# Performance work log

Hardware: AMD Instinct MI355X
Metric: run time of the kernel (lower is better)

## Reference

```python
import jax, jax.numpy as jnp
import numpy as np

OUT, IN = 4096, 4096
PACKED = (OUT * IN + 1) // 2


def setup_inputs() -> dict:
    key = jax.random.key(0)
    k1, k2, k3, k4, k5 = jax.random.split(key, 5)
    x = jax.random.normal(k1, (4, 2048, IN), dtype=jnp.float32)
    weight_packed = jax.random.randint(k2, (PACKED,), 0, 256, dtype=jnp.int32)
    scale = jax.random.uniform(k3, (OUT, 1), dtype=jnp.float32) * 0.01 + 1e-4
    zero_point = jax.random.uniform(k4, (OUT, 1), dtype=jnp.float32) * 8.0
    bias = jax.random.normal(k5, (OUT,), dtype=jnp.float32) * 0.02
    return {"x": x, "weight_packed": weight_packed, "scale": scale,
            "zero_point": zero_point, "bias": bias}


def _dequant_weight(weight_packed, scale, zero_point):
    # Unpack two 4-bit nibbles per byte; low nibble first (matches torch.stack dim=1 + flatten)
    low = (weight_packed & 15).astype(jnp.float32)          # [PACKED]
    high = ((weight_packed >> 4) & 15).astype(jnp.float32)   # [PACKED]
    unpacked = jnp.stack([low, high], axis=1).reshape(-1)     # [2*PACKED]
    w = unpacked[: OUT * IN].reshape(OUT, IN)
    # weight * scale - zero_point * scale == (weight - zero_point) * scale
    return (w - zero_point) * scale                           # [OUT, IN]


def reference(x, weight_packed, scale, zero_point, bias):
    w = _dequant_weight(weight_packed, scale, zero_point)
    # F.linear: x @ w.T + bias
    return jnp.einsum('bsi,oi->bso', x, w) + bias
```

## Files before the change

### kernel.cpp

```cpp
#include <hip/hip_runtime.h>
#include <hip/hip_bf16.h>


typedef __bf16 bf16;
typedef __attribute__((ext_vector_type(8))) __bf16 bf16x8;
typedef __attribute__((ext_vector_type(4))) float f32x4;
typedef __attribute__((ext_vector_type(4))) unsigned int u32x4;

#define OUT_DIM 4096
#define IN_DIM  4096
#define M_DIM   8192

__global__ __launch_bounds__(256) void dequant_w_kernel(
    const int* __restrict__ wp, const float* __restrict__ scale,
    const float* __restrict__ zp, bf16* __restrict__ W)
{
  const int t = blockIdx.x * 256 + threadIdx.x;
  const long j = (long)t * 8;
  const int o = (int)(j >> 12);
  const float s = scale[o];
  const float zs = zp[o] * s;
  const int4 p = *(const int4*)(wp + (long)t * 4);
  const int v[4] = {p.x, p.y, p.z, p.w};
  union { bf16 h[8]; u32x4 u; } r;
#pragma unroll
  for (int q = 0; q < 4; ++q) {
    r.h[2*q]   = (bf16)((float)(v[q] & 15) * s - zs);
    r.h[2*q+1] = (bf16)((float)((v[q] >> 4) & 15) * s - zs);
  }
  *(u32x4*)(W + j) = r.u;
}

__global__ __launch_bounds__(256) void cvt_x_kernel(
    const float* __restrict__ x, bf16* __restrict__ xb)
{
  const long t = (long)blockIdx.x * 256 + threadIdx.x;
  const long i = t * 8;
  const f32x4 a = *(const f32x4*)(x + i);
  const f32x4 b = *(const f32x4*)(x + i + 4);
  union { bf16 h[8]; u32x4 u; } r;
#pragma unroll
  for (int q = 0; q < 4; ++q) { r.h[q] = (bf16)a[q]; r.h[4+q] = (bf16)b[q]; }
  *(u32x4*)(xb + i) = r.u;
}

__global__ __launch_bounds__(512, 2) void gemm_bt_bias_kernel(
    const bf16* __restrict__ A, const bf16* __restrict__ B,
    const float* __restrict__ bias, float* __restrict__ C)
{
  const int N = OUT_DIM, K = IN_DIM;
  const int NT = IN_DIM / 64;

  __shared__ bf16 sm[2][4][256][32];

  const int bid = blockIdx.x;
  const int swz = (bid & 7) * (512 / 8) + (bid >> 3);
  const int bm = swz >> 4;
  const int bn = swz & 15;

  const int tid  = threadIdx.x;
  const int wave = tid >> 6;
  const int lane = tid & 63;
  const int wr = wave >> 2;
  const int wc = wave & 3;

  const long row0 = (long)bm * 256;
  const long col0 = (long)bn * 256;

  const int L0 = tid * 16;
  const int L1 = 8192 + tid * 16;
  const int Lw0 = L0 ^ (((L0 >> 9) & 1) << 5);
  const int Lw1 = L1 ^ (((L1 >> 9) & 1) << 5);
  const int sr0 = Lw0 >> 6, sc0 = (Lw0 & 63) >> 1;
  const int sr1 = Lw1 >> 6, sc1 = (Lw1 & 63) >> 1;
  const bf16* a0 = A + (row0 + sr0) * (long)K + sc0;
  const bf16* a1 = A + (row0 + sr1) * (long)K + sc1;
  const bf16* b0 = B + (col0 + sr0) * (long)K + sc0;
  const bf16* b1 = B + (col0 + sr1) * (long)K + sc1;

#define STAGE(P0, P1, HALF, KOFF) do {                                          \
    __builtin_amdgcn_global_load_lds(                                           \
        (const __attribute__((address_space(1))) void*)((P0) + (KOFF)),         \
        (__attribute__((address_space(3))) void*)((char*)(HALF) + L0), 16, 0, 0);\
    __builtin_amdgcn_global_load_lds(                                           \
        (const __attribute__((address_space(1))) void*)((P1) + (KOFF)),         \
        (__attribute__((address_space(3))) void*)((char*)(HALF) + L1), 16, 0, 0);\
  } while (0)

  const int lane15 = lane & 15;
  const int rb = (lane15 * 64 + ((lane >> 4) << 4)) ^ ((lane & 8) << 2);
  const int wrB = wr * 8192;
  const int wcB = wc * 4096;

  f32x4 acc[8][4] = {};

#define PHASE(BUF, KS, STAGE_STMT, VM_STMT) do {                                \
    VM_STMT;                                                                    \
    __builtin_amdgcn_s_barrier();                                               \
    asm volatile("" ::: "memory");            \
    const char* Ab = (const char*)&sm[BUF][KS][0][0];                           \
    const char* Bb = (const char*)&sm[BUF][2 + (KS)][0][0];                     \
    bf16x8 fb[4], fa[8];                                                        \
    _Pragma("unroll")                                                           \
    for (int f = 0; f < 4; ++f) fb[f] = *(const bf16x8*)(Bb + wcB + f*1024 + rb); \
    _Pragma("unroll")                                                           \
    for (int f = 0; f < 8; ++f) fa[f] = *(const bf16x8*)(Ab + wrB + f*1024 + rb); \
    STAGE_STMT;                                                                 \
    __builtin_amdgcn_s_setprio(1);                                              \
    _Pragma("unroll")                                                           \
    for (int i = 0; i < 8; ++i)                                                 \
      _Pragma("unroll")                                                         \
      for (int j = 0; j < 4; ++j)                                               \
        acc[i][j] = __builtin_amdgcn_mfma_f32_16x16x32_bf16(fa[i], fb[j], acc[i][j], 0, 0, 0); \
    __builtin_amdgcn_s_setprio(0);                                              \
  } while (0)

  STAGE(a0, a1, &sm[0][0][0][0], 0);
  STAGE(b0, b1, &sm[0][2][0][0], 0);
  STAGE(a0, a1, &sm[0][1][0][0], 32);
  STAGE(b0, b1, &sm[0][3][0][0], 32);

  for (int T = 0; T < NT; ++T) {
    const int buf = T & 1;
    const int nbuf = buf ^ 1;
    const int nko = (T + 1) * 64;
    const bool st = (T + 1 < NT);

    PHASE(buf, 0,
          { if (st) { STAGE(a0, a1, &sm[nbuf][0][0][0], nko);
                      STAGE(b0, b1, &sm[nbuf][2][0][0], nko); } },
          { asm volatile("s_waitcnt vmcnt(4)" ::: "memory"); });
    PHASE(buf, 1,
          { if (st) { STAGE(a0, a1, &sm[nbuf][1][0][0], nko + 32);
                      STAGE(b0, b1, &sm[nbuf][3][0][0], nko + 32); } },
          { if (T == NT - 1) asm volatile("s_waitcnt vmcnt(0)" ::: "memory");
            else             asm volatile("s_waitcnt vmcnt(4)" ::: "memory"); });
  }

  const long cr0 = row0 + wr * 128 + ((lane >> 4) << 2);
  const long cc0 = col0 + wc * 64 + lane15;
#pragma unroll
  for (int j = 0; j < 4; ++j) {
    const long gc = cc0 + j * 16;
    const float bv = bias[gc];
#pragma unroll
    for (int mf = 0; mf < 8; ++mf) {
      float* cp = C + (cr0 + mf * 16) * (long)N + gc;
#pragma unroll
      for (int r = 0; r < 4; ++r)
        cp[(long)r * N] = acc[mf][j][r] + bv;
    }
  }
#undef PHASE
#undef STAGE
}

extern "C" void kernel_launch(void* const* d_in, const int* in_sizes, int n_in,
                              void* d_out, int out_size, void* d_ws, size_t ws_size,
                              hipStream_t stream)
{
  const float* x     = (const float*)d_in[0];
  const int*   wp    = (const int*)d_in[1];
  const float* scale = (const float*)d_in[2];
  const float* zp    = (const float*)d_in[3];
  const float* bias  = (const float*)d_in[4];
  float* out = (float*)d_out;

  bf16* Wb = (bf16*)d_ws;
  bf16* Xb = (bf16*)((char*)d_ws + (size_t)OUT_DIM * IN_DIM * 2);

  dequant_w_kernel<<<(OUT_DIM * (long)IN_DIM / 8) / 256, 256, 0, stream>>>(wp, scale, zp, Wb);
  cvt_x_kernel<<<(M_DIM * (long)IN_DIM / 8) / 256, 256, 0, stream>>>(x, Xb);
  gemm_bt_bias_kernel<<<512, 512, 0, stream>>>(Xb, Wb, bias, out);
}
```

Before: 281.9 us.

## Software-pipeline LDS fragment reads with register double-buffering in GEMM loop

The GEMM main loop now reads the next half-tile's A/B fragments from LDS into a second register set while MFMAs run on the current set. Global-to-LDS staging is rescheduled so each half-buffer is refilled as soon as its fragments have been read. The aim is to hide LDS read latency behind the matrix instructions. The extra fragment registers raise register pressure, which could hurt occupancy under the 512x2 launch bounds.

```diff
diff --git a/kernel.cpp b/kernel.cpp
--- a/kernel.cpp
+++ b/kernel.cpp
@@ -93,25 +93,25 @@
   const int wcB = wc * 4096;
 
   f32x4 acc[8][4] = {};
+  bf16x8 pa[8], pb[4];
+  bf16x8 qa[8], qb[4];
 
-#define PHASE(BUF, KS, STAGE_STMT, VM_STMT) do {                                \
-    VM_STMT;                                                                    \
-    __builtin_amdgcn_s_barrier();                                               \
-    asm volatile("" ::: "memory");            \
+#define RD(RA, RB, BUF, KS) do {                                                \
     const char* Ab = (const char*)&sm[BUF][KS][0][0];                           \
     const char* Bb = (const char*)&sm[BUF][2 + (KS)][0][0];                     \
-    bf16x8 fb[4], fa[8];                                                        \
     _Pragma("unroll")                                                           \
-    for (int f = 0; f < 4; ++f) fb[f] = *(const bf16x8*)(Bb + wcB + f*1024 + rb); \
+    for (int f = 0; f < 4; ++f) RB[f] = *(const bf16x8*)(Bb + wcB + f*1024 + rb); \
     _Pragma("unroll")                                                           \
-    for (int f = 0; f < 8; ++f) fa[f] = *(const bf16x8*)(Ab + wrB + f*1024 + rb); \
-    STAGE_STMT;                                                                 \
+    for (int f = 0; f < 8; ++f) RA[f] = *(const bf16x8*)(Ab + wrB + f*1024 + rb); \
+  } while (0)
+
+#define MFMAS(CA, CB) do {                                                      \
     __builtin_amdgcn_s_setprio(1);                                              \
     _Pragma("unroll")                                                           \
     for (int i = 0; i < 8; ++i)                                                 \
       _Pragma("unroll")                                                         \
       for (int j = 0; j < 4; ++j)                                               \
-        acc[i][j] = __builtin_amdgcn_mfma_f32_16x16x32_bf16(fa[i], fb[j], acc[i][j], 0, 0, 0); \
+        acc[i][j] = __builtin_amdgcn_mfma_f32_16x16x32_bf16(CA[i], CB[j], acc[i][j], 0, 0, 0); \
     __builtin_amdgcn_s_setprio(0);                                              \
   } while (0)
 
@@ -119,22 +119,37 @@
   STAGE(b0, b1, &sm[0][2][0][0], 0);
   STAGE(a0, a1, &sm[0][1][0][0], 32);
   STAGE(b0, b1, &sm[0][3][0][0], 32);
+  asm volatile("s_waitcnt vmcnt(4)" ::: "memory");
+  __builtin_amdgcn_s_barrier();
+  STAGE(a0, a1, &sm[1][0][0][0], 64);
+  STAGE(b0, b1, &sm[1][2][0][0], 64);
+  RD(pa, pb, 0, 0);
 
   for (int T = 0; T < NT; ++T) {
     const int buf = T & 1;
     const int nbuf = buf ^ 1;
-    const int nko = (T + 1) * 64;
-    const bool st = (T + 1 < NT);
+    const bool st1 = (T + 1 < NT);
+    const bool st2 = (T + 2 < NT);
 
-    PHASE(buf, 0,
-          { if (st) { STAGE(a0, a1, &sm[nbuf][0][0][0], nko);
-                      STAGE(b0, b1, &sm[nbuf][2][0][0], nko); } },
-          { asm volatile("s_waitcnt vmcnt(4)" ::: "memory"); });
-    PHASE(buf, 1,
-          { if (st) { STAGE(a0, a1, &sm[nbuf][1][0][0], nko + 32);
-                      STAGE(b0, b1, &sm[nbuf][3][0][0], nko + 32); } },
-          { if (T == NT - 1) asm volatile("s_waitcnt vmcnt(0)" ::: "memory");
-            else             asm volatile("s_waitcnt vmcnt(4)" ::: "memory"); });
+    if (st1) asm volatile("s_waitcnt vmcnt(4)" ::: "memory");
+    else     asm volatile("s_waitcnt vmcnt(0)" ::: "memory");
+    __builtin_amdgcn_s_barrier();
+    if (st1) {
+      STAGE(a0, a1, &sm[nbuf][1][0][0], (T + 1) * 64 + 32);
+      STAGE(b0, b1, &sm[nbuf][3][0][0], (T + 1) * 64 + 32);
+    }
+    RD(qa, qb, buf, 1);
+    MFMAS(pa, pb);
+
+    if (st1) asm volatile("s_waitcnt vmcnt(4)" ::: "memory");
+    else     asm volatile("s_waitcnt vmcnt(0)" ::: "memory");
+    __builtin_amdgcn_s_barrier();
+    if (st2) {
+      STAGE(a0, a1, &sm[buf][0][0][0], (T + 2) * 64);
+      STAGE(b0, b1, &sm[buf][2][0][0], (T + 2) * 64);
+    }
+    if (st1) RD(pa, pb, nbuf, 0);
+    MFMAS(qa, qb);
   }
 
   const long cr0 = row0 + wr * 128 + ((lane >> 4) << 2);
@@ -151,7 +166,8 @@
         cp[(long)r * N] = acc[mf][j][r] + bv;
     }
   }
-#undef PHASE
+#undef RD
+#undef MFMAS
 #undef STAGE
 }
 
```

Result: slower. 291.4 us (+3.4%).

## Fuse weight dequantization into GEMM with packed 4-bit LDS staging

Applied to the files above, without the earlier changes.

Removes the standalone bf16 weight dequant kernel. A small repack kernel now compresses the int32-per-byte weights into dense packed bytes. The GEMM loads those 4-bit nibbles into LDS with 4-byte global_load_lds and dequantizes them to bf16 fragments in registers, using per-column scale and zero-point held in registers, just before the MFMAs. This cuts weight write/read traffic and LDS footprint, at the cost of extra VALU work in the MFMA inner loop. That unpack work is also repeated by the waves that share the same columns.

```diff
diff --git a/kernel.cpp b/kernel.cpp
--- a/kernel.cpp
+++ b/kernel.cpp
@@ -10,26 +10,6 @@
 #define OUT_DIM 4096
 #define IN_DIM  4096
 #define M_DIM   8192
-
-__global__ __launch_bounds__(256) void dequant_w_kernel(
-    const int* __restrict__ wp, const float* __restrict__ scale,
-    const float* __restrict__ zp, bf16* __restrict__ W)
-{
-  const int t = blockIdx.x * 256 + threadIdx.x;
-  const long j = (long)t * 8;
-  const int o = (int)(j >> 12);
-  const float s = scale[o];
-  const float zs = zp[o] * s;
-  const int4 p = *(const int4*)(wp + (long)t * 4);
-  const int v[4] = {p.x, p.y, p.z, p.w};
-  union { bf16 h[8]; u32x4 u; } r;
-#pragma unroll
-  for (int q = 0; q < 4; ++q) {
-    r.h[2*q]   = (bf16)((float)(v[q] & 15) * s - zs);
-    r.h[2*q+1] = (bf16)((float)((v[q] >> 4) & 15) * s - zs);
-  }
-  *(u32x4*)(W + j) = r.u;
-}
 
 __global__ __launch_bounds__(256) void cvt_x_kernel(
     const float* __restrict__ x, bf16* __restrict__ xb)
@@ -44,14 +24,31 @@
   *(u32x4*)(xb + i) = r.u;
 }
 
+__global__ __launch_bounds__(256) void repack_w_kernel(
+    const int* __restrict__ wp, unsigned int* __restrict__ wb)
+{
+  const long t = (long)blockIdx.x * 256 + threadIdx.x;
+  const long e = t * 16;
+  u32x4 r;
+#pragma unroll
+  for (int q = 0; q < 4; ++q) {
+    const int4 p = *(const int4*)(wp + e + q * 4);
+    r[q] = (unsigned)(p.x & 255) | ((unsigned)(p.y & 255) << 8) |
+           ((unsigned)(p.z & 255) << 16) | ((unsigned)(p.w & 255) << 24);
+  }
+  *(u32x4*)(wb + t * 4) = r;
+}
+
 __global__ __launch_bounds__(512, 2) void gemm_bt_bias_kernel(
-    const bf16* __restrict__ A, const bf16* __restrict__ B,
+    const bf16* __restrict__ A, const unsigned char* __restrict__ WP,
+    const float* __restrict__ scale, const float* __restrict__ zp,
     const float* __restrict__ bias, float* __restrict__ C)
 {
   const int N = OUT_DIM, K = IN_DIM;
   const int NT = IN_DIM / 64;
 
-  __shared__ bf16 sm[2][4][256][32];
+  __shared__ bf16 smA[2][2][256][32];
+  __shared__ unsigned int smB[2][2][256][4];
 
   const int bid = blockIdx.x;
   const int swz = (bid & 7) * (512 / 8) + (bid >> 3);
@@ -75,37 +72,65 @@
   const int sr1 = Lw1 >> 6, sc1 = (Lw1 & 63) >> 1;
   const bf16* a0 = A + (row0 + sr0) * (long)K + sc0;
   const bf16* a1 = A + (row0 + sr1) * (long)K + sc1;
-  const bf16* b0 = B + (col0 + sr0) * (long)K + sc0;
-  const bf16* b1 = B + (col0 + sr1) * (long)K + sc1;
 
-#define STAGE(P0, P1, HALF, KOFF) do {                                          \
+  const int brow  = tid >> 2;
+  const int bbyte = (tid & 3) * 4;
+  const unsigned char* w0 = WP + (col0 + brow) * 2048L + bbyte;
+  const unsigned char* w1 = WP + (col0 + brow + 128) * 2048L + bbyte;
+
+#define STAGE_G(BUF, KS, KOFF) do {                                             \
+    char* Ah = (char*)&smA[BUF][KS][0][0];                                      \
+    char* Bh = (char*)&smB[BUF][KS][0][0];                                      \
     __builtin_amdgcn_global_load_lds(                                           \
-        (const __attribute__((address_space(1))) void*)((P0) + (KOFF)),         \
-        (__attribute__((address_space(3))) void*)((char*)(HALF) + L0), 16, 0, 0);\
+        (const __attribute__((address_space(1))) void*)(a0 + (KOFF)),           \
+        (__attribute__((address_space(3))) void*)(Ah + L0), 16, 0, 0);          \
     __builtin_amdgcn_global_load_lds(                                           \
-        (const __attribute__((address_space(1))) void*)((P1) + (KOFF)),         \
-        (__attribute__((address_space(3))) void*)((char*)(HALF) + L1), 16, 0, 0);\
+        (const __attribute__((address_space(1))) void*)(a1 + (KOFF)),           \
+        (__attribute__((address_space(3))) void*)(Ah + L1), 16, 0, 0);          \
+    __builtin_amdgcn_global_load_lds(                                           \
+        (const __attribute__((address_space(1))) void*)(w0 + ((KOFF) >> 1)),    \
+        (__attribute__((address_space(3))) void*)(Bh + tid * 4), 4, 0, 0);      \
+    __builtin_amdgcn_global_load_lds(                                           \
+        (const __attribute__((address_space(1))) void*)(w1 + ((KOFF) >> 1)),    \
+        (__attribute__((address_space(3))) void*)(Bh + 2048 + tid * 4), 4, 0, 0);\
   } while (0)
 
   const int lane15 = lane & 15;
-  const int rb = (lane15 * 64 + ((lane >> 4) << 4)) ^ ((lane & 8) << 2);
+  const int rb  = (lane15 * 64 + ((lane >> 4) << 4)) ^ ((lane & 8) << 2);
   const int wrB = wr * 8192;
-  const int wcB = wc * 4096;
+  const int rBb = (wc * 64 + lane15) * 16 + ((lane >> 4) << 2);
+
+  float sv[4], zv[4];
+#pragma unroll
+  for (int f = 0; f < 4; ++f) {
+    const int n = (int)col0 + wc * 64 + f * 16 + lane15;
+    sv[f] = scale[n];
+    zv[f] = zp[n] * sv[f];
+  }
 
   f32x4 acc[8][4] = {};
 
 #define PHASE(BUF, KS, STAGE_STMT, VM_STMT) do {                                \
     VM_STMT;                                                                    \
     __builtin_amdgcn_s_barrier();                                               \
-    asm volatile("" ::: "memory");            \
-    const char* Ab = (const char*)&sm[BUF][KS][0][0];                           \
-    const char* Bb = (const char*)&sm[BUF][2 + (KS)][0][0];                     \
-    bf16x8 fb[4], fa[8];                                                        \
+    asm volatile("" ::: "memory");        \
+    const char* Ab = (const char*)&smA[BUF][KS][0][0];                          \
+    const char* Bp = (const char*)&smB[BUF][KS][0][0];                          \
+    unsigned int pk[4];                                                         \
     _Pragma("unroll")                                                           \
-    for (int f = 0; f < 4; ++f) fb[f] = *(const bf16x8*)(Bb + wcB + f*1024 + rb); \
+    for (int f = 0; f < 4; ++f) pk[f] = *(const unsigned int*)(Bp + rBb + f * 256); \
+    bf16x8 fa[8];                                                               \
     _Pragma("unroll")                                                           \
-    for (int f = 0; f < 8; ++f) fa[f] = *(const bf16x8*)(Ab + wrB + f*1024 + rb); \
+    for (int f = 0; f < 8; ++f) fa[f] = *(const bf16x8*)(Ab + wrB + f * 1024 + rb); \
     STAGE_STMT;                                                                 \
+    bf16x8 fb[4];                                                               \
+    _Pragma("unroll")                                                           \
+    for (int f = 0; f < 4; ++f) {                                               \
+      const float fs = sv[f], fz = zv[f];                                       \
+      _Pragma("unroll")                                                         \
+      for (int e = 0; e < 8; ++e)                                               \
+        fb[f][e] = (bf16)((float)((pk[f] >> (4 * e)) & 15u) * fs - fz);         \
+    }                                                                           \
     __builtin_amdgcn_s_setprio(1);                                              \
     _Pragma("unroll")                                                           \
     for (int i = 0; i < 8; ++i)                                                 \
@@ -115,10 +140,8 @@
     __builtin_amdgcn_s_setprio(0);                                              \
   } while (0)
 
-  STAGE(a0, a1, &sm[0][0][0][0], 0);
-  STAGE(b0, b1, &sm[0][2][0][0], 0);
-  STAGE(a0, a1, &sm[0][1][0][0], 32);
-  STAGE(b0, b1, &sm[0][3][0][0], 32);
+  STAGE_G(0, 0, 0);
+  STAGE_G(0, 1, 32);
 
   for (int T = 0; T < NT; ++T) {
     const int buf = T & 1;
@@ -127,12 +150,10 @@
     const bool st = (T + 1 < NT);
 
     PHASE(buf, 0,
-          { if (st) { STAGE(a0, a1, &sm[nbuf][0][0][0], nko);
-                      STAGE(b0, b1, &sm[nbuf][2][0][0], nko); } },
+          { if (st) STAGE_G(nbuf, 0, nko); },
           { asm volatile("s_waitcnt vmcnt(4)" ::: "memory"); });
     PHASE(buf, 1,
-          { if (st) { STAGE(a0, a1, &sm[nbuf][1][0][0], nko + 32);
-                      STAGE(b0, b1, &sm[nbuf][3][0][0], nko + 32); } },
+          { if (st) STAGE_G(nbuf, 1, nko + 32); },
           { if (T == NT - 1) asm volatile("s_waitcnt vmcnt(0)" ::: "memory");
             else             asm volatile("s_waitcnt vmcnt(4)" ::: "memory"); });
   }
@@ -152,7 +173,7 @@
     }
   }
 #undef PHASE
-#undef STAGE
+#undef STAGE_G
 }
 
 extern "C" void kernel_launch(void* const* d_in, const int* in_sizes, int n_in,
@@ -166,10 +187,11 @@
   const float* bias  = (const float*)d_in[4];
   float* out = (float*)d_out;
 
-  bf16* Wb = (bf16*)d_ws;
-  bf16* Xb = (bf16*)((char*)d_ws + (size_t)OUT_DIM * IN_DIM * 2);
+  bf16* Xb = (bf16*)d_ws;
+  unsigned int* Wb = (unsigned int*)((char*)d_ws + 67108864);
 
-  dequant_w_kernel<<<(OUT_DIM * (long)IN_DIM / 8) / 256, 256, 0, stream>>>(wp, scale, zp, Wb);
   cvt_x_kernel<<<(M_DIM * (long)IN_DIM / 8) / 256, 256, 0, stream>>>(x, Xb);
-  gemm_bt_bias_kernel<<<512, 512, 0, stream>>>(Xb, Wb, bias, out);
+  repack_w_kernel<<<(OUT_DIM * (long)IN_DIM / 2 / 16) / 256, 256, 0, stream>>>(wp, Wb);
+  gemm_bt_bias_kernel<<<512, 512, 0, stream>>>(
+      Xb, (const unsigned char*)Wb, scale, zp, bias, out);
 }
```

Result: slower. 335.1 us (+18.9%).

## Switch GEMM to 32x32x16 bf16 MFMA with matching LDS tile layout

Applied to the files above, without the earlier changes.

Replaces the 16x16x32 MFMA tiling with 32x32x16 bf16 MFMA instructions, so each wave holds a 4x2 grid of 32x32 accumulators instead of 8x4 16x16 tiles. The global-to-LDS staging layout and fragment addressing are rewritten so lanes read the operand layout the larger MFMA expects, and the epilogue store mapping is adjusted to match. The larger MFMA issues fewer instructions and reads fewer LDS fragments per FLOP. The new LDS layout drops the previous XOR swizzle, which risks LDS bank conflicts on the fragment reads.

```diff
diff --git a/kernel.cpp b/kernel.cpp
--- a/kernel.cpp
+++ b/kernel.cpp
@@ -5,6 +5,7 @@
 typedef __bf16 bf16;
 typedef __attribute__((ext_vector_type(8))) __bf16 bf16x8;
 typedef __attribute__((ext_vector_type(4))) float f32x4;
+typedef __attribute__((ext_vector_type(16))) float f32x16;
 typedef __attribute__((ext_vector_type(4))) unsigned int u32x4;
 
 #define OUT_DIM 4096
@@ -51,7 +52,8 @@
   const int N = OUT_DIM, K = IN_DIM;
   const int NT = IN_DIM / 64;
 
-  __shared__ bf16 sm[2][4][256][32];
+  __shared__ char smA[2][2][16384];
+  __shared__ char smB[2][2][16384];
 
   const int bid = blockIdx.x;
   const int swz = (bid & 7) * (512 / 8) + (bid >> 3);
@@ -59,66 +61,73 @@
   const int bn = swz & 15;
 
   const int tid  = threadIdx.x;
+  const int lane = tid & 63;
   const int wave = tid >> 6;
-  const int lane = tid & 63;
   const int wr = wave >> 2;
   const int wc = wave & 3;
 
   const long row0 = (long)bm * 256;
   const long col0 = (long)bn * 256;
 
-  const int L0 = tid * 16;
-  const int L1 = 8192 + tid * 16;
-  const int Lw0 = L0 ^ (((L0 >> 9) & 1) << 5);
-  const int Lw1 = L1 ^ (((L1 >> 9) & 1) << 5);
-  const int sr0 = Lw0 >> 6, sc0 = (Lw0 & 63) >> 1;
-  const int sr1 = Lw1 >> 6, sc1 = (Lw1 & 63) >> 1;
-  const bf16* a0 = A + (row0 + sr0) * (long)K + sc0;
-  const bf16* a1 = A + (row0 + sr1) * (long)K + sc1;
-  const bf16* b0 = B + (col0 + sr0) * (long)K + sc0;
-  const bf16* b1 = B + (col0 + sr1) * (long)K + sc1;
+  const int arow = (tid >> 7) * 32 + (tid & 31);
+  const int kadj = ((tid >> 6) & 1) * 16 + ((tid >> 5) & 1) * 8;
+  const bf16* aP0 = A + (row0 + arow) * (long)K + kadj;
+  const bf16* aP1 = aP0 + 128 * (long)K;
+  const bf16* bP0 = B + (col0 + arow) * (long)K + kadj;
+  const bf16* bP1 = bP0 + 128 * (long)K;
+  const int LA = tid * 16;
 
-#define STAGE(P0, P1, HALF, KOFF) do {                                          \
-    __builtin_amdgcn_global_load_lds(                                           \
-        (const __attribute__((address_space(1))) void*)((P0) + (KOFF)),         \
-        (__attribute__((address_space(3))) void*)((char*)(HALF) + L0), 16, 0, 0);\
-    __builtin_amdgcn_global_load_lds(                                           \
-        (const __attribute__((address_space(1))) void*)((P1) + (KOFF)),         \
-        (__attribute__((address_space(3))) void*)((char*)(HALF) + L1), 16, 0, 0);\
+#define GL(P, D) __builtin_amdgcn_global_load_lds(                              \
+      (const __attribute__((address_space(1))) void*)(P),                       \
+      (__attribute__((address_space(3))) void*)(D), 16, 0, 0)
+
+#define STAGE_G(BUF, KS, KOFF) do {                                             \
+    char* Ah = &smA[BUF][KS][0];                                                \
+    char* Bh = &smB[BUF][KS][0];                                                \
+    GL(aP0 + (KOFF), Ah + LA);                                                  \
+    GL(aP1 + (KOFF), Ah + 8192 + LA);                                           \
+    GL(bP0 + (KOFF), Bh + LA);                                                  \
+    GL(bP1 + (KOFF), Bh + 8192 + LA);                                           \
   } while (0)
 
-  const int lane15 = lane & 15;
-  const int rb = (lane15 * 64 + ((lane >> 4) << 4)) ^ ((lane & 8) << 2);
-  const int wrB = wr * 8192;
-  const int wcB = wc * 4096;
+  const int laneoff = ((lane >> 5) << 9) + ((lane & 31) << 4);
+  const int waB = wr * 4 * 2048;
+  const int wbB = wc * 2 * 2048;
 
-  f32x4 acc[8][4] = {};
+  f32x16 acc[4][2] = {};
 
 #define PHASE(BUF, KS, STAGE_STMT, VM_STMT) do {                                \
     VM_STMT;                                                                    \
     __builtin_amdgcn_s_barrier();                                               \
-    asm volatile("" ::: "memory");            \
-    const char* Ab = (const char*)&sm[BUF][KS][0][0];                           \
-    const char* Bb = (const char*)&sm[BUF][2 + (KS)][0][0];                     \
-    bf16x8 fb[4], fa[8];                                                        \
+    asm volatile("" ::: "memory");        \
+    const char* Ab = &smA[BUF][KS][0];                                          \
+    const char* Bb = &smB[BUF][KS][0];                                          \
+    bf16x8 fb[2][2], fa[4][2];                                                  \
     _Pragma("unroll")                                                           \
-    for (int f = 0; f < 4; ++f) fb[f] = *(const bf16x8*)(Bb + wcB + f*1024 + rb); \
+    for (int n = 0; n < 2; ++n)                                                 \
+      _Pragma("unroll")                                                         \
+      for (int kk = 0; kk < 2; ++kk)                                            \
+        fb[n][kk] = *(const bf16x8*)(Bb + wbB + n * 2048 + kk * 1024 + laneoff);\
     _Pragma("unroll")                                                           \
-    for (int f = 0; f < 8; ++f) fa[f] = *(const bf16x8*)(Ab + wrB + f*1024 + rb); \
+    for (int m = 0; m < 4; ++m)                                                 \
+      _Pragma("unroll")                                                         \
+      for (int kk = 0; kk < 2; ++kk)                                            \
+        fa[m][kk] = *(const bf16x8*)(Ab + waB + m * 2048 + kk * 1024 + laneoff);\
     STAGE_STMT;                                                                 \
     __builtin_amdgcn_s_setprio(1);                                              \
     _Pragma("unroll")                                                           \
-    for (int i = 0; i < 8; ++i)                                                 \
+    for (int kk = 0; kk < 2; ++kk)                                              \
       _Pragma("unroll")                                                         \
-      for (int j = 0; j < 4; ++j)                                               \
-        acc[i][j] = __builtin_amdgcn_mfma_f32_16x16x32_bf16(fa[i], fb[j], acc[i][j], 0, 0, 0); \
+      for (int m = 0; m < 4; ++m)                                               \
+        _Pragma("unroll")                                                       \
+        for (int n = 0; n < 2; ++n)                                             \
+          acc[m][n] = __builtin_amdgcn_mfma_f32_32x32x16_bf16(                  \
+              fa[m][kk], fb[n][kk], acc[m][n], 0, 0, 0);                        \
     __builtin_amdgcn_s_setprio(0);                                              \
   } while (0)
 
-  STAGE(a0, a1, &sm[0][0][0][0], 0);
-  STAGE(b0, b1, &sm[0][2][0][0], 0);
-  STAGE(a0, a1, &sm[0][1][0][0], 32);
-  STAGE(b0, b1, &sm[0][3][0][0], 32);
+  STAGE_G(0, 0, 0);
+  STAGE_G(0, 1, 32);
 
   for (int T = 0; T < NT; ++T) {
     const int buf = T & 1;
@@ -127,32 +136,37 @@
     const bool st = (T + 1 < NT);
 
     PHASE(buf, 0,
-          { if (st) { STAGE(a0, a1, &sm[nbuf][0][0][0], nko);
-                      STAGE(b0, b1, &sm[nbuf][2][0][0], nko); } },
+          { if (st) STAGE_G(nbuf, 0, nko); },
           { asm volatile("s_waitcnt vmcnt(4)" ::: "memory"); });
     PHASE(buf, 1,
-          { if (st) { STAGE(a0, a1, &sm[nbuf][1][0][0], nko + 32);
-                      STAGE(b0, b1, &sm[nbuf][3][0][0], nko + 32); } },
+          { if (st) STAGE_G(nbuf, 1, nko + 32); },
           { if (T == NT - 1) asm volatile("s_waitcnt vmcnt(0)" ::: "memory");
             else             asm volatile("s_waitcnt vmcnt(4)" ::: "memory"); });
   }
 
-  const long cr0 = row0 + wr * 128 + ((lane >> 4) << 2);
-  const long cc0 = col0 + wc * 64 + lane15;
+  const int l31 = lane & 31;
+  const int hi4 = (lane >> 5) * 4;
+  const long cr0 = row0 + wr * 128 + hi4;
+  float bv[2];
 #pragma unroll
-  for (int j = 0; j < 4; ++j) {
-    const long gc = cc0 + j * 16;
-    const float bv = bias[gc];
+  for (int n = 0; n < 2; ++n) bv[n] = bias[col0 + wc * 64 + n * 32 + l31];
 #pragma unroll
-    for (int mf = 0; mf < 8; ++mf) {
-      float* cp = C + (cr0 + mf * 16) * (long)N + gc;
+  for (int n = 0; n < 2; ++n) {
+    const long gc = col0 + wc * 64 + n * 32 + l31;
 #pragma unroll
-      for (int r = 0; r < 4; ++r)
-        cp[(long)r * N] = acc[mf][j][r] + bv;
+    for (int m = 0; m < 4; ++m) {
+#pragma unroll
+      for (int q = 0; q < 4; ++q) {
+        float* cp = C + (cr0 + m * 32 + q * 8) * (long)N + gc;
+#pragma unroll
+        for (int j = 0; j < 4; ++j)
+          cp[(long)j * N] = acc[m][n][q * 4 + j] + bv[n];
+      }
     }
   }
 #undef PHASE
-#undef STAGE
+#undef STAGE_G
+#undef GL
 }
 
 extern "C" void kernel_launch(void* const* d_in, const int* in_sizes, int n_in,
```

New measurement: 327.2 us. 1.16x slower.
